# Performance work log

Hardware: AMD Instinct MI355X
Metric: run time of the kernel (lower is better)

## Reference

```python
import jax, jax.numpy as jnp
import numpy as np

B, N, L = 8, 170, 336
PATCH = 16
P = L // PATCH            # 21 patches, pad_len = 0
D_MODEL = 128
D_STATE = 16
D_CONV = 4
D_INNER = 2 * D_MODEL     # expand=2
DT_RANK = 8               # ceil(d_model/16)
PRED_LEN = 96


def setup_inputs() -> dict:
    key = jax.random.key(0)
    ks = jax.random.split(key, 16)
    def nrm(k, shape, s=0.02):
        return jax.random.normal(k, shape, jnp.float32) * s
    return {
        "x": jax.random.normal(ks[0], (B, N, L), jnp.float32),
        "node_embed_map": nrm(ks[1], (1, N, 1, D_MODEL)),
        "pe_W": nrm(ks[2], (D_MODEL, PATCH), 0.1),
        "pe_b": jnp.zeros((D_MODEL,), jnp.float32),
        "pos_emb": nrm(ks[3], (1, 1, P, D_MODEL)),
        "r_W1": nrm(ks[4], (D_MODEL // 4, 3), 0.3),
        "r_b1": jnp.zeros((D_MODEL // 4,), jnp.float32),
        "r_W2": nrm(ks[5], (D_MODEL, D_MODEL // 4), 0.1),
        "r_b2": jnp.zeros((D_MODEL,), jnp.float32),
        "ln_g": jnp.ones((D_MODEL,), jnp.float32),
        "ln_b": jnp.zeros((D_MODEL,), jnp.float32),
        "in_proj_W": nrm(ks[6], (2 * D_INNER, D_MODEL), 0.05),
        "conv_W": nrm(ks[7], (D_INNER, D_CONV), 0.2),
        "conv_b": jnp.zeros((D_INNER,), jnp.float32),
        "x_proj_W": nrm(ks[8], (DT_RANK + 2 * D_STATE, D_INNER), 0.05),
        "dt_proj_W": nrm(ks[9], (D_INNER, DT_RANK), 0.3),
        "dt_proj_b": nrm(ks[10], (D_INNER,), 0.5),
        "A_log": jnp.log(jnp.broadcast_to(jnp.arange(1.0, D_STATE + 1.0, dtype=jnp.float32), (D_INNER, D_STATE))),
        "D_skip": jnp.ones((D_INNER,), jnp.float32),
        "out_proj_W": nrm(ks[11], (D_MODEL, D_INNER), 0.05),
        "head_W": nrm(ks[12], (PRED_LEN, P * D_MODEL), 0.02),
        "head_b": jnp.zeros((PRED_LEN,), jnp.float32),
    }


def _layernorm(x, g, b, eps=1e-5):
    mu = x.mean(-1, keepdims=True)
    var = ((x - mu) ** 2).mean(-1, keepdims=True)
    return (x - mu) * jax.lax.rsqrt(var + eps) * g + b


def _router(x_patch, r_W1, r_b1, r_W2, r_b2):
    # FFT energy over each length-16 patch -> low/mid/high band features -> tiny MLP gate
    X = jnp.fft.rfft(x_patch, axis=-1)          # [M, P, 9]
    energy = X.real ** 2 + X.imag ** 2
    fl = energy.shape[-1]
    s1, s2 = fl // 3, 2 * fl // 3
    feats = jnp.stack([energy[..., :s1].sum(-1),
                       energy[..., s1:s2].sum(-1),
                       energy[..., s2:].sum(-1)], axis=-1)
    feats = feats / (feats.sum(-1, keepdims=True) + 1e-6)
    h = jax.nn.relu(feats @ r_W1.T + r_b1)
    return jax.nn.sigmoid(h @ r_W2.T + r_b2)    # [M, P, d_model]


def _mamba(u, in_proj_W, conv_W, conv_b, x_proj_W, dt_proj_W, dt_proj_b, A_log, D_skip, out_proj_W):
    # u: [M, T, d_model]  (Mamba block: in_proj -> causal dwconv -> SSM scan -> gate -> out_proj)
    M, T, _ = u.shape
    xz = u @ in_proj_W.T                        # [M, T, 2*d_inner]
    xc, z = jnp.split(xz, 2, axis=-1)
    # causal depthwise conv1d, kernel D_CONV
    xp = jnp.pad(xc, ((0, 0), (D_CONV - 1, 0), (0, 0)))
    conv = conv_b + sum(xp[:, k:k + T, :] * conv_W[:, k] for k in range(D_CONV))
    xs = jax.nn.silu(conv)                      # [M, T, d_inner]
    proj = xs @ x_proj_W.T                      # [M, T, dt_rank + 2*d_state]
    dt_in = proj[..., :DT_RANK]
    Bm = proj[..., DT_RANK:DT_RANK + D_STATE]
    Cm = proj[..., DT_RANK + D_STATE:]
    dt = jax.nn.softplus(dt_in @ dt_proj_W.T + dt_proj_b)  # [M, T, d_inner]
    A = -jnp.exp(A_log)                         # [d_inner, d_state]

    def step(h, inp):
        dt_t, B_t, C_t, u_t = inp               # [M,d_inner], [M,d_state], [M,d_state], [M,d_inner]
        dA = jnp.exp(dt_t[..., None] * A)       # [M, d_inner, d_state]
        h = dA * h + (dt_t * u_t)[..., None] * B_t[:, None, :]
        y = jnp.einsum('mds,ms->md', h, C_t)
        return h, y

    h0 = jnp.zeros((M, D_INNER, D_STATE), jnp.float32)
    _, ys = jax.lax.scan(step, h0, (jnp.moveaxis(dt, 1, 0), jnp.moveaxis(Bm, 1, 0),
                                    jnp.moveaxis(Cm, 1, 0), jnp.moveaxis(xs, 1, 0)))
    y = jnp.moveaxis(ys, 0, 1) + xs * D_skip
    y = y * jax.nn.silu(z)
    return y @ out_proj_W.T


def reference(x, node_embed_map, pe_W, pe_b, pos_emb, r_W1, r_b1, r_W2, r_b2,
              ln_g, ln_b, in_proj_W, conv_W, conv_b, x_proj_W, dt_proj_W, dt_proj_b,
              A_log, D_skip, out_proj_W, head_W, head_b):
    Bb, Nn, _ = x.shape
    x_patches = x.reshape(Bb, Nn, P, PATCH)                     # pad_len == 0 for L=336
    x_enc = x_patches @ pe_W.T + pe_b + pos_emb + node_embed_map
    x_enc_flat = x_enc.reshape(Bb * Nn, P, D_MODEL)
    gate = _router(x_patches.reshape(Bb * Nn, P, PATCH), r_W1, r_b1, r_W2, r_b2)
    x_gated = _layernorm(x_enc_flat, ln_g, ln_b) * gate
    y = _mamba(x_gated, in_proj_W, conv_W, conv_b, x_proj_W, dt_proj_W, dt_proj_b,
               A_log, D_skip, out_proj_W)
    out = (y + x_enc_flat).reshape(Bb, Nn, P * D_MODEL)         # dropout is identity (eval)
    return out @ head_W.T + head_b                              # [B, N, pred_len]
```

## Files before the change

### kernel.cpp

```cpp
#include <hip/hip_runtime.h>
#include <math.h>

#define B_ 8
#define N_ 170
#define L_ 336
#define PATCH_ 16
#define P_ 21
#define DM_ 128
#define DS_ 16
#define DI_ 256
#define PL_ 96
#define M_ (B_ * N_)
#define T_ 21
#define R_ (M_ * T_)
#define KF_ (P_ * DM_)

typedef __attribute__((ext_vector_type(8))) short short8;
typedef __attribute__((ext_vector_type(4))) float f32x4;

__device__ inline unsigned short f2b(float f) {
    unsigned int u = __builtin_bit_cast(unsigned int, f);
    u += 0x7fff + ((u >> 16) & 1);
    return (unsigned short)(u >> 16);
}
__device__ inline float b2f(unsigned short h) {
    unsigned int u = ((unsigned int)h) << 16;
    return __builtin_bit_cast(float, u);
}
__device__ inline float fast_sigmoid(float v) {
    return __builtin_amdgcn_rcpf(1.f + __expf(-v));
}

__global__ __launch_bounds__(256) void k_convert(
    const float* __restrict__ inW, const float* __restrict__ xpW,
    const float* __restrict__ outW, const float* __restrict__ hW,
    const float* __restrict__ peW, const float* __restrict__ rW2,
    unsigned short* __restrict__ winb, unsigned short* __restrict__ wxpb,
    unsigned short* __restrict__ woutb, unsigned short* __restrict__ whb,
    unsigned short* __restrict__ peWb, unsigned short* __restrict__ rW2b)
{
    int i = blockIdx.x * 256 + threadIdx.x;
    if (i < 65536) { winb[i] = f2b(inW[i]); return; }
    i -= 65536;
    if (i < 16384) {
        int j = i >> 8;
        wxpb[i] = (j < 40) ? f2b(xpW[j * 256 + (i & 255)]) : (unsigned short)0;
        return;
    }
    i -= 16384;
    if (i < 32768) { woutb[i] = f2b(outW[i]); return; }
    i -= 32768;
    if (i < 258048) { whb[i] = f2b(hW[i]); return; }
    i -= 258048;
    if (i < 4096) {
        int r = i >> 5, j = i & 31;
        peWb[i] = (j < 16) ? f2b(peW[r * 16 + j]) : (unsigned short)0;
        return;
    }
    i -= 4096;
    if (i < 4096) { rW2b[i] = f2b(rW2[i]); }
}

__global__ __launch_bounds__(256) void k_fused(
    const float* __restrict__ x, const float* __restrict__ nem,
    const unsigned short* __restrict__ peWb, const float* __restrict__ peB,
    const float* __restrict__ posE,
    const float* __restrict__ rW1, const float* __restrict__ rB1,
    const unsigned short* __restrict__ rW2b, const float* __restrict__ rB2,
    const float* __restrict__ lnG, const float* __restrict__ lnB,
    const unsigned short* __restrict__ winb,
    const float* __restrict__ convW, const float* __restrict__ convB,
    const unsigned short* __restrict__ wxpb,
    const float* __restrict__ dtW, const float* __restrict__ dtB,
    const float* __restrict__ Dsk,
    const unsigned short* __restrict__ woutb,
    unsigned short* __restrict__ feat)
{
    __shared__ __align__(16) char lds[36896];
    unsigned short* xencs = (unsigned short*)(lds + 0);
    unsigned short* us    = (unsigned short*)(lds + 5552);
    unsigned short* zsl   = (unsigned short*)(lds + 5552);
    unsigned short* xss   = (unsigned short*)(lds + 16640);
    float*          pjs   = (float*)(lds + 33536);
    float*          xls   = (float*)(lds + 14256);
    float*          ctst  = (float*)(lds + 15600);
    unsigned short* pa    = (unsigned short*)(lds + 15728);
    unsigned short* ha    = (unsigned short*)(lds + 18288);
    float*          es    = (float*)(lds + 20848);
    unsigned short* gs    = (unsigned short*)(lds + 21608);
    float*          pn    = (float*)(lds + 27160);
    unsigned short* posEs = (unsigned short*)(lds + 27672);

    const int m = blockIdx.x;
    const int n = m % N_;
    const int tid = threadIdx.x;
    const int lane = tid & 63;
    const int w = tid >> 6;
    const int lo = lane & 15, kq = (lane >> 4) * 8;
    const int rl = (lane >> 4) * 4, cl = lane & 15;

    for (int i = tid; i < L_; i += 256) xls[i] = x[m * L_ + i];
    for (int i = tid; i < 32 * 40; i += 256) {
        const int p = i / 40, j = i - p * 40;
        pa[i] = (p < P_ && j < PATCH_) ? f2b(x[m * L_ + p * PATCH_ + j])
                                       : (unsigned short)0;
        ha[i] = 0;
    }
    if (tid < 16) {
        float s, c;
        sincosf((float)tid * (6.283185307179586f / 16.f), &s, &c);
        ctst[tid] = c; ctst[16 + tid] = s;
    }
    if (tid >= 64 && tid < 192) pn[tid - 64] = peB[tid - 64] + nem[n * DM_ + tid - 64];
    for (int i = tid; i < P_ * DM_; i += 256)
        posEs[(i >> 7) * 132 + (i & 127)] = f2b(posE[i]);
    {
        int* usI = (int*)us;
        for (int i = tid; i < 11 * 68; i += 256) usI[21 * 68 + i] = 0;
    }
    __syncthreads();

    for (int i = tid; i < P_ * 9; i += 256) {
        const int p = i / 9, bin = i - p * 9;
        const float* xp = &xls[p * PATCH_];
        float re = 0.f, im = 0.f;
#pragma unroll
        for (int j = 0; j < PATCH_; ++j) {
            int idx = (bin * j) & 15;
            re = fmaf(xp[j], ctst[idx], re);
            im = fmaf(xp[j], -ctst[16 + idx], im);
        }
        es[i] = re * re + im * im;
    }
    __syncthreads();

    for (int idx = tid; idx < P_ * 32; idx += 256) {
        const int p = idx >> 5, i = idx & 31;
        const float* e = &es[p * 9];
        float b0 = e[0] + e[1] + e[2];
        float b1 = e[3] + e[4] + e[5];
        float b2 = e[6] + e[7] + e[8];
        float inv = __builtin_amdgcn_rcpf(b0 + b1 + b2 + 1e-6f);
        float hv = rB1[i];
        hv = fmaf(b0 * inv, rW1[i * 3 + 0], hv);
        hv = fmaf(b1 * inv, rW1[i * 3 + 1], hv);
        hv = fmaf(b2 * inv, rW1[i * 3 + 2], hv);
        ha[p * 40 + i] = f2b(hv > 0.f ? hv : 0.f);
    }
    {
        const unsigned short* bb = peWb + (w * 32 + lo) * 32 + kq;
        short8 b0 = *(const short8*)bb;
        short8 b1 = *(const short8*)(bb + 16 * 32);
        short8 a0 = *(const short8*)&pa[lo * 40 + kq];
        short8 a1 = *(const short8*)&pa[(16 + lo) * 40 + kq];
        f32x4 z = {0.f, 0.f, 0.f, 0.f};
        f32x4 C[2][2];
        C[0][0] = __builtin_amdgcn_mfma_f32_16x16x32_bf16(a0, b0, z, 0, 0, 0);
        C[0][1] = __builtin_amdgcn_mfma_f32_16x16x32_bf16(a0, b1, z, 0, 0, 0);
        C[1][0] = __builtin_amdgcn_mfma_f32_16x16x32_bf16(a1, b0, z, 0, 0, 0);
        C[1][1] = __builtin_amdgcn_mfma_f32_16x16x32_bf16(a1, b1, z, 0, 0, 0);
#pragma unroll
        for (int mi = 0; mi < 2; ++mi)
#pragma unroll
            for (int r = 0; r < 4; ++r) {
                const int row = mi * 16 + rl + r;
                if (row < P_) {
#pragma unroll
                    for (int ni = 0; ni < 2; ++ni) {
                        const int col = w * 32 + ni * 16 + cl;
                        float xe = C[mi][ni][r] + pn[col] + b2f(posEs[row * 132 + col]);
                        xencs[row * 132 + col] = f2b(xe);
                    }
                }
            }
    }
    __syncthreads();

    {
        const unsigned short* bb = rW2b + (w * 32 + lo) * 32 + kq;
        short8 b0 = *(const short8*)bb;
        short8 b1 = *(const short8*)(bb + 16 * 32);
        short8 a0 = *(const short8*)&ha[lo * 40 + kq];
        short8 a1 = *(const short8*)&ha[(16 + lo) * 40 + kq];
        f32x4 z = {0.f, 0.f, 0.f, 0.f};
        f32x4 C[2][2];
        C[0][0] = __builtin_amdgcn_mfma_f32_16x16x32_bf16(a0, b0, z, 0, 0, 0);
        C[0][1] = __builtin_amdgcn_mfma_f32_16x16x32_bf16(a0, b1, z, 0, 0, 0);
        C[1][0] = __builtin_amdgcn_mfma_f32_16x16x32_bf16(a1, b0, z, 0, 0, 0);
        C[1][1] = __builtin_amdgcn_mfma_f32_16x16x32_bf16(a1, b1, z, 0, 0, 0);
#pragma unroll
        for (int mi = 0; mi < 2; ++mi)
#pragma unroll
            for (int r = 0; r < 4; ++r) {
                const int row = mi * 16 + rl + r;
                if (row < P_) {
#pragma unroll
                    for (int ni = 0; ni < 2; ++ni) {
                        const int col = w * 32 + ni * 16 + cl;
                        gs[row * 132 + col] = f2b(fast_sigmoid(C[mi][ni][r] + rB2[col]));
                    }
                }
            }
    }
    __syncthreads();

    {
        const float lg0 = lnG[lane], lg1 = lnG[lane + 64];
        const float lb0 = lnB[lane], lb1 = lnB[lane + 64];
        for (int it = 0; it < 6; ++it) {
            const int p = it * 4 + w;
            if (p >= P_) continue;
            float xe0 = b2f(xencs[p * 132 + lane]);
            float xe1 = b2f(xencs[p * 132 + 64 + lane]);
            float g0 = b2f(gs[p * 132 + lane]);
            float g1 = b2f(gs[p * 132 + 64 + lane]);
            float s = xe0 + xe1, s2 = xe0 * xe0 + xe1 * xe1;
#pragma unroll
            for (int off = 32; off; off >>= 1) {
                s += __shfl_xor(s, off);
                s2 += __shfl_xor(s2, off);
            }
            float mu = s * (1.f / 128.f);
            float var = s2 * (1.f / 128.f) - mu * mu;
            float rs = rsqrtf(var + 1e-5f);
            us[p * 136 + lane]      = f2b(((xe0 - mu) * rs * lg0 + lb0) * g0);
            us[p * 136 + 64 + lane] = f2b(((xe1 - mu) * rs * lg1 + lb1) * g1);
        }
    }
    __syncthreads();

    {
        f32x4 C[2][8];
#pragma unroll
        for (int mi = 0; mi < 2; ++mi)
#pragma unroll
            for (int ni = 0; ni < 8; ++ni) C[mi][ni] = (f32x4){0.f, 0.f, 0.f, 0.f};

        const unsigned short* bbase = winb + (size_t)(w * 128 + lo) * DM_ + kq;
#pragma unroll
        for (int k0 = 0; k0 < DM_; k0 += 32) {
            short8 a0 = *(const short8*)&us[lo * 136 + k0 + kq];
            short8 a1 = *(const short8*)&us[(16 + lo) * 136 + k0 + kq];
#pragma unroll
            for (int ni = 0; ni < 8; ++ni) {
                short8 b = *(const short8*)(bbase + ni * 16 * DM_ + k0);
                C[0][ni] = __builtin_amdgcn_mfma_f32_16x16x32_bf16(a0, b, C[0][ni], 0, 0, 0);
                C[1][ni] = __builtin_amdgcn_mfma_f32_16x16x32_bf16(a1, b, C[1][ni], 0, 0, 0);
            }
        }
        __syncthreads();

        {
            int* xsI = (int*)xss;
            for (int i = tid; i < 11 * 132; i += 256) xsI[21 * 132 + i] = 0;
        }
        const int cbase = (w & 1) * 128 + cl;
        if (w < 2) {
#pragma unroll
            for (int ni = 0; ni < 8; ++ni) {
                const int col = cbase + ni * 16;
#pragma unroll
                for (int mi = 0; mi < 2; ++mi)
#pragma unroll
                    for (int r = 0; r < 4; ++r) {
                        const int row = mi * 16 + rl + r;
                        if (row < T_) xss[row * 264 + col] = f2b(C[mi][ni][r]);
                    }
            }
        } else {
#pragma unroll
            for (int ni = 0; ni < 8; ++ni) {
                const int col = cbase + ni * 16;
#pragma unroll
                for (int mi = 0; mi < 2; ++mi)
#pragma unroll
                    for (int r = 0; r < 4; ++r) {
                        const int row = mi * 16 + rl + r;
                        if (row < T_) {
                            float v = C[mi][ni][r];
                            zsl[row * 264 + col] = f2b(v * fast_sigmoid(v));
                        }
                    }
            }
        }
    }
    __syncthreads();

    {
        const int d = tid;
        float4 cw = *(const float4*)(convW + d * 4);
        const float cb = convB[d];
        float c0 = 0.f, c1 = 0.f, c2 = 0.f;
#pragma unroll
        for (int t = 0; t < T_; ++t) {
            float c3 = b2f(xss[t * 264 + d]);
            float v = cb;
            v = fmaf(c0, cw.x, v);
            v = fmaf(c1, cw.y, v);
            v = fmaf(c2, cw.z, v);
            v = fmaf(c3, cw.w, v);
            v = v * fast_sigmoid(v);
            xss[t * 264 + d] = f2b(v);
            c0 = c1; c1 = c2; c2 = c3;
        }
    }
    __syncthreads();

    {
        const int mt = w >> 1, nt = w & 1;
        const unsigned short* ar = &xss[(mt * 16 + lo) * 264 + kq];
        const unsigned short* bp0 = wxpb + (nt * 32 + lo) * DI_ + kq;
        const unsigned short* bp1 = bp0 + 16 * DI_;
        f32x4 c0 = {0.f, 0.f, 0.f, 0.f}, c1 = c0;
#pragma unroll
        for (int k0 = 0; k0 < DI_; k0 += 32) {
            short8 a  = *(const short8*)(ar + k0);
            short8 b0 = *(const short8*)(bp0 + k0);
            short8 b1 = *(const short8*)(bp1 + k0);
            c0 = __builtin_amdgcn_mfma_f32_16x16x32_bf16(a, b0, c0, 0, 0, 0);
            c1 = __builtin_amdgcn_mfma_f32_16x16x32_bf16(a, b1, c1, 0, 0, 0);
        }
#pragma unroll
        for (int r = 0; r < 4; ++r) {
            const int row = mt * 16 + rl + r;
            const int ca = nt * 32 + cl, cb = ca + 16;
            if (row < T_) {
                if (ca < 40) pjs[row * 40 + ca] = c0[r];
                if (cb < 40) pjs[row * 40 + cb] = c1[r];
            }
        }
    }
    __syncthreads();

    {
        const int d = tid;
        float dw[8];
        *(float4*)&dw[0] = *(const float4*)(dtW + d * 8);
        *(float4*)&dw[4] = *(const float4*)(dtW + d * 8 + 4);
        const float db = dtB[d], Dv = Dsk[d];
        const f32x4* pj4 = (const f32x4*)pjs;
        float h[DS_];
#pragma unroll
        for (int s = 0; s < DS_; ++s) h[s] = 0.f;
#pragma unroll
        for (int t = 0; t < T_; ++t) {
            f32x4 d0 = pj4[t * 10 + 0], d1 = pj4[t * 10 + 1];
            f32x4 Bv[4], Cv[4];
#pragma unroll
            for (int q = 0; q < 4; ++q) { Bv[q] = pj4[t * 10 + 2 + q]; Cv[q] = pj4[t * 10 + 6 + q]; }
            float a = db;
#pragma unroll
            for (int r = 0; r < 4; ++r) a = fmaf(d0[r], dw[r], a);
#pragma unroll
            for (int r = 0; r < 4; ++r) a = fmaf(d1[r], dw[4 + r], a);
            float qe = __expf(a);
            float dt = (a > 20.f) ? a : __logf(1.f + qe);
            float e1 = __builtin_amdgcn_rcpf(1.f + qe);
            float ut = b2f(xss[t * 264 + d]);
            float zq = b2f(zsl[t * 264 + d]);
            float wk = dt * ut;
            float dA = 1.f;
            float yv = 0.f;
#pragma unroll
            for (int s = 0; s < DS_; ++s) {
                dA *= e1;
                h[s] = fmaf(dA, h[s], wk * Bv[s >> 2][s & 3]);
                yv = fmaf(h[s], Cv[s >> 2][s & 3], yv);
            }
            yv = fmaf(ut, Dv, yv) * zq;
            xss[t * 264 + d] = f2b(yv);
        }
    }
    __syncthreads();

    {
        f32x4 C[2][2];
#pragma unroll
        for (int mi = 0; mi < 2; ++mi)
#pragma unroll
            for (int ni = 0; ni < 2; ++ni) C[mi][ni] = (f32x4){0.f, 0.f, 0.f, 0.f};

        const unsigned short* bbase = woutb + (size_t)(w * 32 + lo) * DI_ + kq;
#pragma unroll
        for (int k0 = 0; k0 < DI_; k0 += 32) {
            short8 a0 = *(const short8*)&xss[lo * 264 + k0 + kq];
            short8 a1 = *(const short8*)&xss[(16 + lo) * 264 + k0 + kq];
#pragma unroll
            for (int ni = 0; ni < 2; ++ni) {
                short8 b = *(const short8*)(bbase + ni * 16 * DI_ + k0);
                C[0][ni] = __builtin_amdgcn_mfma_f32_16x16x32_bf16(a0, b, C[0][ni], 0, 0, 0);
                C[1][ni] = __builtin_amdgcn_mfma_f32_16x16x32_bf16(a1, b, C[1][ni], 0, 0, 0);
            }
        }
        unsigned short* fb = feat + (size_t)m * T_ * DM_;
#pragma unroll
        for (int mi = 0; mi < 2; ++mi)
#pragma unroll
            for (int r = 0; r < 4; ++r) {
                const int row = mi * 16 + rl + r;
                if (row < T_) {
#pragma unroll
                    for (int ni = 0; ni < 2; ++ni) {
                        const int col = w * 32 + ni * 16 + cl;
                        float res = b2f(xencs[row * 132 + col]);
                        fb[row * DM_ + col] = f2b(C[mi][ni][r] + res);
                    }
                }
            }
    }
}

__global__ __launch_bounds__(256) void k_gemm_head(
    const unsigned short* __restrict__ feat, const unsigned short* __restrict__ W,
    const float* __restrict__ hB, float* __restrict__ out)
{
    __shared__ float red[4 * 512];
    const int bid = blockIdx.x;
    const int wm = bid / 3, wn = bid % 3;
    const int tid = threadIdx.x, w = tid >> 6, lane = tid & 63;
    const int r0 = wm * 16, n0 = wn * 32;
    const int lo = lane & 15, kq = (lane >> 4) * 8;
    const int kb = w * 672;
    const unsigned short* ap  = feat + (size_t)(r0 + lo) * KF_ + kb + kq;
    const unsigned short* bp0 = W + (size_t)(n0 + lo) * KF_ + kb + kq;
    const unsigned short* bp1 = bp0 + 16 * KF_;
    f32x4 c0 = {0.f, 0.f, 0.f, 0.f}, c1 = c0;
#pragma unroll 3
    for (int k0 = 0; k0 < 672; k0 += 32) {
        short8 a  = *(const short8*)(ap + k0);
        short8 b0 = *(const short8*)(bp0 + k0);
        short8 b1 = *(const short8*)(bp1 + k0);
        c0 = __builtin_amdgcn_mfma_f32_16x16x32_bf16(a, b0, c0, 0, 0, 0);
        c1 = __builtin_amdgcn_mfma_f32_16x16x32_bf16(a, b1, c1, 0, 0, 0);
    }
    float* rw = &red[w * 512 + lane * 8];
#pragma unroll
    for (int r = 0; r < 4; ++r) { rw[r] = c0[r]; rw[4 + r] = c1[r]; }
    __syncthreads();

    for (int f = tid; f < 512; f += 256) {
        float s = red[f] + red[512 + f] + red[1024 + f] + red[1536 + f];
        const int l = f >> 3, v = f & 7;
        const int row = r0 + ((l >> 4) << 2) + (v & 3);
        const int col = n0 + (l & 15) + ((v >= 4) ? 16 : 0);
        out[row * PL_ + col] = s + hB[col];
    }
}

extern "C" void kernel_launch(void* const* d_in, const int* in_sizes, int n_in,
                              void* d_out, int out_size, void* d_ws, size_t ws_size,
                              hipStream_t stream)
{
    const float* x     = (const float*)d_in[0];
    const float* nem   = (const float*)d_in[1];
    const float* peW   = (const float*)d_in[2];
    const float* peB   = (const float*)d_in[3];
    const float* posE  = (const float*)d_in[4];
    const float* rW1   = (const float*)d_in[5];
    const float* rB1   = (const float*)d_in[6];
    const float* rW2   = (const float*)d_in[7];
    const float* rB2   = (const float*)d_in[8];
    const float* lnG   = (const float*)d_in[9];
    const float* lnB   = (const float*)d_in[10];
    const float* inW   = (const float*)d_in[11];
    const float* convW = (const float*)d_in[12];
    const float* convB = (const float*)d_in[13];
    const float* xpW   = (const float*)d_in[14];
    const float* dtW   = (const float*)d_in[15];
    const float* dtB   = (const float*)d_in[16];
    const float* Dsk   = (const float*)d_in[18];
    const float* outW  = (const float*)d_in[19];
    const float* hW    = (const float*)d_in[20];
    const float* hB    = (const float*)d_in[21];
    float* out = (float*)d_out;

    char* ws = (char*)d_ws;
    size_t off = 0;
    auto alloc = [&](size_t bytes) { size_t o = off; off = (off + bytes + 255) & ~(size_t)255; return o; };
    unsigned short* feat  = (unsigned short*)(ws + alloc((size_t)R_ * DM_ * 2));
    unsigned short* winb  = (unsigned short*)(ws + alloc(512 * 128 * 2));
    unsigned short* wxpb  = (unsigned short*)(ws + alloc(64 * 256 * 2));
    unsigned short* woutb = (unsigned short*)(ws + alloc(128 * 256 * 2));
    unsigned short* whb   = (unsigned short*)(ws + alloc(96 * KF_ * 2));
    unsigned short* peWb  = (unsigned short*)(ws + alloc(128 * 32 * 2));
    unsigned short* rW2b  = (unsigned short*)(ws + alloc(128 * 32 * 2));

    k_convert<<<1488, 256, 0, stream>>>(inW, xpW, outW, hW, peW, rW2,
                                        winb, wxpb, woutb, whb, peWb, rW2b);
    k_fused<<<M_, 256, 0, stream>>>(x, nem, peWb, peB, posE,
                                    rW1, rB1, rW2b, rB2, lnG, lnB,
                                    winb, convW, convB, wxpb,
                                    dtW, dtB, Dsk, woutb, feat);
    k_gemm_head<<<255, 256, 0, stream>>>(feat, whb, hB, out);
}
```

Measured before the change: 202.3 us.

## Shrink fused kernel LDS footprint and split in_proj into two phases

```diff
diff --git a/kernel.cpp b/kernel.cpp
--- a/kernel.cpp
+++ b/kernel.cpp
@@ -14,6 +14,11 @@
 #define T_ 21
 #define R_ (M_ * T_)
 #define KF_ (P_ * DM_)
+
+#define XST 260
+#define ZST 256
+#define UST2 132
+#define EST 128
 
 typedef __attribute__((ext_vector_type(8))) short short8;
 typedef __attribute__((ext_vector_type(4))) float f32x4;
@@ -76,20 +81,19 @@
     const unsigned short* __restrict__ woutb,
     unsigned short* __restrict__ feat)
 {
-    __shared__ __align__(16) char lds[36896];
-    unsigned short* xencs = (unsigned short*)(lds + 0);
-    unsigned short* us    = (unsigned short*)(lds + 5552);
-    unsigned short* zsl   = (unsigned short*)(lds + 5552);
-    unsigned short* xss   = (unsigned short*)(lds + 16640);
-    float*          pjs   = (float*)(lds + 33536);
-    float*          xls   = (float*)(lds + 14256);
-    float*          ctst  = (float*)(lds + 15600);
-    unsigned short* pa    = (unsigned short*)(lds + 15728);
-    unsigned short* ha    = (unsigned short*)(lds + 18288);
-    float*          es    = (float*)(lds + 20848);
-    unsigned short* gs    = (unsigned short*)(lds + 21608);
-    float*          pn    = (float*)(lds + 27160);
-    unsigned short* posEs = (unsigned short*)(lds + 27672);
+    __shared__ __align__(16) char lds[32592];
+    unsigned short* xss   = (unsigned short*)(lds + 0);
+    unsigned short* zsl   = (unsigned short*)(lds + 10920);
+    unsigned short* usj   = (unsigned short*)(lds + 21840);
+    float*          pjs   = (float*)(lds + 21840);
+    unsigned short* xencs = (unsigned short*)(lds + 27384);
+    unsigned short* gs    = (unsigned short*)(lds + 0);
+    unsigned short* pa    = (unsigned short*)(lds + 5376);
+    unsigned short* ha    = (unsigned short*)(lds + 7936);
+    float*          es    = (float*)(lds + 10496);
+    float*          ctst  = (float*)(lds + 11252);
+    float*          pn    = (float*)(lds + 11380);
+    unsigned short* posEs = (unsigned short*)(lds + 11892);
 
     const int m = blockIdx.x;
     const int n = m % N_;
@@ -99,12 +103,10 @@
     const int lo = lane & 15, kq = (lane >> 4) * 8;
     const int rl = (lane >> 4) * 4, cl = lane & 15;
 
-    for (int i = tid; i < L_; i += 256) xls[i] = x[m * L_ + i];
     for (int i = tid; i < 32 * 40; i += 256) {
         const int p = i / 40, j = i - p * 40;
         pa[i] = (p < P_ && j < PATCH_) ? f2b(x[m * L_ + p * PATCH_ + j])
                                        : (unsigned short)0;
-        ha[i] = 0;
     }
     if (tid < 16) {
         float s, c;
@@ -113,22 +115,19 @@
     }
     if (tid >= 64 && tid < 192) pn[tid - 64] = peB[tid - 64] + nem[n * DM_ + tid - 64];
     for (int i = tid; i < P_ * DM_; i += 256)
-        posEs[(i >> 7) * 132 + (i & 127)] = f2b(posE[i]);
-    {
-        int* usI = (int*)us;
-        for (int i = tid; i < 11 * 68; i += 256) usI[21 * 68 + i] = 0;
-    }
+        posEs[(i >> 7) * EST + (i & 127)] = f2b(posE[i]);
     __syncthreads();
 
     for (int i = tid; i < P_ * 9; i += 256) {
         const int p = i / 9, bin = i - p * 9;
-        const float* xp = &xls[p * PATCH_];
+        const unsigned short* xp = &pa[p * 40];
         float re = 0.f, im = 0.f;
 #pragma unroll
         for (int j = 0; j < PATCH_; ++j) {
             int idx = (bin * j) & 15;
-            re = fmaf(xp[j], ctst[idx], re);
-            im = fmaf(xp[j], -ctst[16 + idx], im);
+            float xv = b2f(xp[j]);
+            re = fmaf(xv, ctst[idx], re);
+            im = fmaf(xv, -ctst[16 + idx], im);
         }
         es[i] = re * re + im * im;
     }
@@ -168,8 +167,8 @@
 #pragma unroll
                     for (int ni = 0; ni < 2; ++ni) {
                         const int col = w * 32 + ni * 16 + cl;
-                        float xe = C[mi][ni][r] + pn[col] + b2f(posEs[row * 132 + col]);
-                        xencs[row * 132 + col] = f2b(xe);
+                        float xe = C[mi][ni][r] + pn[col] + b2f(posEs[row * EST + col]);
+                        xencs[row * EST + col] = f2b(xe);
                     }
                 }
             }
@@ -197,7 +196,7 @@
 #pragma unroll
                     for (int ni = 0; ni < 2; ++ni) {
                         const int col = w * 32 + ni * 16 + cl;
-                        gs[row * 132 + col] = f2b(fast_sigmoid(C[mi][ni][r] + rB2[col]));
+                        gs[row * EST + col] = f2b(fast_sigmoid(C[mi][ni][r] + rB2[col]));
                     }
                 }
             }
@@ -210,10 +209,10 @@
         for (int it = 0; it < 6; ++it) {
             const int p = it * 4 + w;
             if (p >= P_) continue;
-            float xe0 = b2f(xencs[p * 132 + lane]);
-            float xe1 = b2f(xencs[p * 132 + 64 + lane]);
-            float g0 = b2f(gs[p * 132 + lane]);
-            float g1 = b2f(gs[p * 132 + 64 + lane]);
+            float xe0 = b2f(xencs[p * EST + lane]);
+            float xe1 = b2f(xencs[p * EST + 64 + lane]);
+            float g0 = b2f(gs[p * EST + lane]);
+            float g1 = b2f(gs[p * EST + 64 + lane]);
             float s = xe0 + xe1, s2 = xe0 * xe0 + xe1 * xe1;
 #pragma unroll
             for (int off = 32; off; off >>= 1) {
@@ -223,54 +222,48 @@
             float mu = s * (1.f / 128.f);
             float var = s2 * (1.f / 128.f) - mu * mu;
             float rs = rsqrtf(var + 1e-5f);
-            us[p * 136 + lane]      = f2b(((xe0 - mu) * rs * lg0 + lb0) * g0);
-            us[p * 136 + 64 + lane] = f2b(((xe1 - mu) * rs * lg1 + lb1) * g1);
-        }
-    }
-    __syncthreads();
-
-    {
-        f32x4 C[2][8];
+            usj[p * UST2 + lane]      = f2b(((xe0 - mu) * rs * lg0 + lb0) * g0);
+            usj[p * UST2 + 64 + lane] = f2b(((xe1 - mu) * rs * lg1 + lb1) * g1);
+        }
+    }
+    __syncthreads();
+
+    for (int ph = 0; ph < 2; ++ph) {
+        f32x4 C[2][4];
 #pragma unroll
         for (int mi = 0; mi < 2; ++mi)
 #pragma unroll
-            for (int ni = 0; ni < 8; ++ni) C[mi][ni] = (f32x4){0.f, 0.f, 0.f, 0.f};
-
-        const unsigned short* bbase = winb + (size_t)(w * 128 + lo) * DM_ + kq;
+            for (int ni = 0; ni < 4; ++ni) C[mi][ni] = (f32x4){0.f, 0.f, 0.f, 0.f};
+
+        const unsigned short* bbase = winb + (size_t)(w * 128 + ph * 64 + lo) * DM_ + kq;
 #pragma unroll
         for (int k0 = 0; k0 < DM_; k0 += 32) {
-            short8 a0 = *(const short8*)&us[lo * 136 + k0 + kq];
-            short8 a1 = *(const short8*)&us[(16 + lo) * 136 + k0 + kq];
-#pragma unroll
-            for (int ni = 0; ni < 8; ++ni) {
+            short8 a0 = *(const short8*)&usj[lo * UST2 + k0 + kq];
+            short8 a1 = *(const short8*)&usj[(16 + lo) * UST2 + k0 + kq];
+#pragma unroll
+            for (int ni = 0; ni < 4; ++ni) {
                 short8 b = *(const short8*)(bbase + ni * 16 * DM_ + k0);
                 C[0][ni] = __builtin_amdgcn_mfma_f32_16x16x32_bf16(a0, b, C[0][ni], 0, 0, 0);
                 C[1][ni] = __builtin_amdgcn_mfma_f32_16x16x32_bf16(a1, b, C[1][ni], 0, 0, 0);
             }
         }
-        __syncthreads();
-
-        {
-            int* xsI = (int*)xss;
-            for (int i = tid; i < 11 * 132; i += 256) xsI[21 * 132 + i] = 0;
-        }
-        const int cbase = (w & 1) * 128 + cl;
+        const int cb0 = (w & 1) * 128 + ph * 64 + cl;
         if (w < 2) {
 #pragma unroll
-            for (int ni = 0; ni < 8; ++ni) {
-                const int col = cbase + ni * 16;
+            for (int ni = 0; ni < 4; ++ni) {
+                const int col = cb0 + ni * 16;
 #pragma unroll
                 for (int mi = 0; mi < 2; ++mi)
 #pragma unroll
                     for (int r = 0; r < 4; ++r) {
                         const int row = mi * 16 + rl + r;
-                        if (row < T_) xss[row * 264 + col] = f2b(C[mi][ni][r]);
+                        if (row < T_) xss[row * XST + col] = f2b(C[mi][ni][r]);
                     }
             }
         } else {
 #pragma unroll
-            for (int ni = 0; ni < 8; ++ni) {
-                const int col = cbase + ni * 16;
+            for (int ni = 0; ni < 4; ++ni) {
+                const int col = cb0 + ni * 16;
 #pragma unroll
                 for (int mi = 0; mi < 2; ++mi)
 #pragma unroll
@@ -278,7 +271,7 @@
                         const int row = mi * 16 + rl + r;
                         if (row < T_) {
                             float v = C[mi][ni][r];
-                            zsl[row * 264 + col] = f2b(v * fast_sigmoid(v));
+                            zsl[row * ZST + col] = f2b(v * fast_sigmoid(v));
                         }
                     }
             }
@@ -293,14 +286,14 @@
         float c0 = 0.f, c1 = 0.f, c2 = 0.f;
 #pragma unroll
         for (int t = 0; t < T_; ++t) {
-            float c3 = b2f(xss[t * 264 + d]);
+            float c3 = b2f(xss[t * XST + d]);
             float v = cb;
             v = fmaf(c0, cw.x, v);
             v = fmaf(c1, cw.y, v);
             v = fmaf(c2, cw.z, v);
             v = fmaf(c3, cw.w, v);
             v = v * fast_sigmoid(v);
-            xss[t * 264 + d] = f2b(v);
+            xss[t * XST + d] = f2b(v);
             c0 = c1; c1 = c2; c2 = c3;
         }
     }
@@ -308,7 +301,7 @@
 
     {
         const int mt = w >> 1, nt = w & 1;
-        const unsigned short* ar = &xss[(mt * 16 + lo) * 264 + kq];
+        const unsigned short* ar = &xss[(mt * 16 + lo) * XST + kq];
         const unsigned short* bp0 = wxpb + (nt * 32 + lo) * DI_ + kq;
         const unsigned short* bp1 = bp0 + 16 * DI_;
         f32x4 c0 = {0.f, 0.f, 0.f, 0.f}, c1 = c0;
@@ -356,8 +349,8 @@
             float qe = __expf(a);
             float dt = (a > 20.f) ? a : __logf(1.f + qe);
             float e1 = __builtin_amdgcn_rcpf(1.f + qe);
-            float ut = b2f(xss[t * 264 + d]);
-            float zq = b2f(zsl[t * 264 + d]);
+            float ut = b2f(xss[t * XST + d]);
+            float zq = b2f(zsl[t * ZST + d]);
             float wk = dt * ut;
             float dA = 1.f;
             float yv = 0.f;
@@ -368,7 +361,7 @@
                 yv = fmaf(h[s], Cv[s >> 2][s & 3], yv);
             }
             yv = fmaf(ut, Dv, yv) * zq;
-            xss[t * 264 + d] = f2b(yv);
+            xss[t * XST + d] = f2b(yv);
         }
     }
     __syncthreads();
@@ -383,8 +376,8 @@
         const unsigned short* bbase = woutb + (size_t)(w * 32 + lo) * DI_ + kq;
 #pragma unroll
         for (int k0 = 0; k0 < DI_; k0 += 32) {
-            short8 a0 = *(const short8*)&xss[lo * 264 + k0 + kq];
-            short8 a1 = *(const short8*)&xss[(16 + lo) * 264 + k0 + kq];
+            short8 a0 = *(const short8*)&xss[lo * XST + k0 + kq];
+            short8 a1 = *(const short8*)&xss[(16 + lo) * XST + k0 + kq];
 #pragma unroll
             for (int ni = 0; ni < 2; ++ni) {
                 short8 b = *(const short8*)(bbase + ni * 16 * DI_ + k0);
@@ -402,7 +395,7 @@
 #pragma unroll
                     for (int ni = 0; ni < 2; ++ni) {
                         const int col = w * 32 + ni * 16 + cl;
-                        float res = b2f(xencs[row * 132 + col]);
+                        float res = b2f(xencs[row * EST + col]);
                         fb[row * DM_ + col] = f2b(C[mi][ni][r] + res);
                     }
                 }
```

Measured after the change: 191.8 us. 1.05x faster.
